# Performance work log

Hardware: AMD Instinct MI355X
Metric: run time of the kernel (lower is better)

Reference implementation:

```python
import jax, jax.numpy as jnp
import numpy as np

TEMPERATURE = 0.07
EPS = 1e-12  # F.normalize eps


def _l2norm(x):
    n = jnp.sqrt(jnp.sum(x * x, axis=-1, keepdims=True))
    return x / jnp.maximum(n, EPS)


def _nce_dir(v, x, temp):
    # Faithful to the source's bug: for every anchor k, the negative pool is the
    # FIRST N entries of the flattened (i, j!=i) negsim list, i.e.
    # sim(v0, x_j) for j=1..N-1 followed by sim(v1, x_0).
    pos = jnp.sum(v * x, axis=-1) / temp          # (N,) diagonal sims
    row0 = (v[0] @ x.T) / temp                    # (N,) sims of v0 vs all x
    extra = (v[1] @ x[0]) / temp                  # scalar: sim(v1, x0)
    sum_neg = jnp.sum(jnp.exp(row0[1:])) + jnp.exp(extra)  # fixed across k
    loss = jnp.log(jnp.exp(pos) + sum_neg) - pos  # log(sumexp_all) - log(exp_pos)
    loss = jnp.where(jnp.isnan(loss), jnp.zeros_like(loss), loss)
    return jnp.mean(loss)


def setup_inputs() -> dict:
    key = jax.random.key(0)
    k1, k2, k3 = jax.random.split(key, 3)
    N, D = 16384, 1024
    return {
        "v_f": jax.random.normal(k1, (N, D), dtype=jnp.float32),
        "a_f": jax.random.normal(k2, (N, D), dtype=jnp.float32),
        "t_f": jax.random.normal(k3, (N, D), dtype=jnp.float32),
    }


def reference(v_f, a_f, t_f):
    v = _l2norm(v_f)
    a = _l2norm(a_f)
    t = _l2norm(t_f)
    loss_va = _nce_dir(v, a, TEMPERATURE)
    loss_vt = _nce_dir(v, t, TEMPERATURE)
    return (loss_va, loss_vt)
```

## Files before the change

### kernel.cpp

```cpp
#include <hip/hip_runtime.h>
#include <math.h>

#define D_DIM 1024
#define TEMP_INV 14.285714285714286f
#define L2EPS 1e-12f

typedef float f32x4 __attribute__((ext_vector_type(4)));


__device__ __forceinline__ float dot4(const f32x4 p, const f32x4 q) {
    return p.x*q.x + p.y*q.y + p.z*q.z + p.w*q.w;
}

__global__ __launch_bounds__(256) void nce_rowstats(
    const float* __restrict__ v, const float* __restrict__ a,
    const float* __restrict__ t, float* __restrict__ ws, int N)
{
    __shared__ f32x4 v0s[256];
    const int tid  = threadIdx.x;
    const int wave = tid >> 6;
    const int lane = tid & 63;
    const int row  = blockIdx.x * 4 + wave;

    v0s[tid] = ((const f32x4*)v)[tid];
    __syncthreads();

    if (row >= N) return;

    const f32x4* vr = (const f32x4*)(v + (size_t)row * D_DIM);
    const f32x4* ar = (const f32x4*)(a + (size_t)row * D_DIM);
    const f32x4* tr = (const f32x4*)(t + (size_t)row * D_DIM);

    const f32x4 V0 = __builtin_nontemporal_load(vr + lane      );
    const f32x4 V1 = __builtin_nontemporal_load(vr + lane +  64);
    const f32x4 V2 = __builtin_nontemporal_load(vr + lane + 128);
    const f32x4 V3 = __builtin_nontemporal_load(vr + lane + 192);
    const f32x4 A0 = __builtin_nontemporal_load(ar + lane      );
    const f32x4 A1 = __builtin_nontemporal_load(ar + lane +  64);
    const f32x4 A2 = __builtin_nontemporal_load(ar + lane + 128);
    const f32x4 A3 = __builtin_nontemporal_load(ar + lane + 192);
    const f32x4 T0 = __builtin_nontemporal_load(tr + lane      );
    const f32x4 T1 = __builtin_nontemporal_load(tr + lane +  64);
    const f32x4 T2 = __builtin_nontemporal_load(tr + lane + 128);
    const f32x4 T3 = __builtin_nontemporal_load(tr + lane + 192);

    const f32x4 Z0 = v0s[lane      ];
    const f32x4 Z1 = v0s[lane +  64];
    const f32x4 Z2 = v0s[lane + 128];
    const f32x4 Z3 = v0s[lane + 192];

    float sv  = dot4(V0,V0) + dot4(V1,V1) + dot4(V2,V2) + dot4(V3,V3);
    float sa  = dot4(A0,A0) + dot4(A1,A1) + dot4(A2,A2) + dot4(A3,A3);
    float st  = dot4(T0,T0) + dot4(T1,T1) + dot4(T2,T2) + dot4(T3,T3);
    float dva = dot4(V0,A0) + dot4(V1,A1) + dot4(V2,A2) + dot4(V3,A3);
    float dvt = dot4(V0,T0) + dot4(V1,T1) + dot4(V2,T2) + dot4(V3,T3);
    float d0a = dot4(Z0,A0) + dot4(Z1,A1) + dot4(Z2,A2) + dot4(Z3,A3);
    float d0t = dot4(Z0,T0) + dot4(Z1,T1) + dot4(Z2,T2) + dot4(Z3,T3);

    #pragma unroll
    for (int off = 32; off >= 1; off >>= 1) {
        sv  += __shfl_down(sv,  off);
        sa  += __shfl_down(sa,  off);
        st  += __shfl_down(st,  off);
        dva += __shfl_down(dva, off);
        dvt += __shfl_down(dvt, off);
        d0a += __shfl_down(d0a, off);
        d0t += __shfl_down(d0t, off);
    }

    if (lane == 0) {
        ws[0*N + row] = sqrtf(sv);
        ws[1*N + row] = sqrtf(sa);
        ws[2*N + row] = sqrtf(st);
        ws[3*N + row] = dva;
        ws[4*N + row] = dvt;
        ws[5*N + row] = d0a;
        ws[6*N + row] = d0t;
    }
}

__device__ __forceinline__ void block_reduce2_256(float& x, float& y, float* sred) {
    const int lane = threadIdx.x & 63;
    const int wave = threadIdx.x >> 6;
    #pragma unroll
    for (int off = 32; off >= 1; off >>= 1) {
        x += __shfl_down(x, off);
        y += __shfl_down(y, off);
    }
    if (lane == 0) { sred[wave] = x; sred[4 + wave] = y; }
    __syncthreads();
    if (threadIdx.x == 0) {
        x = sred[0] + sred[1] + sred[2] + sred[3];
        y = sred[4] + sred[5] + sred[6] + sred[7];
    }
}

__global__ __launch_bounds__(256) void nce_partials(
    const float* __restrict__ v, const float* __restrict__ a,
    const float* __restrict__ t, float* __restrict__ ws, int N)
{
    __shared__ float sred[8];
    const int tid = threadIdx.x;
    const int bid = blockIdx.x;
    const size_t B = 7 * (size_t)N;

    float r1 = 0.f, r2 = 0.f;
    if (bid < 32) {
        const float nv0 = fmaxf(ws[0], L2EPS);
        #pragma unroll
        for (int k = 0; k < 2; ++k) {
            const int j = bid * 512 + k * 256 + tid;
            if (j == 0) continue;
            const float ia = 1.0f / (nv0 * fmaxf(ws[1*N + j], L2EPS));
            const float it = 1.0f / (nv0 * fmaxf(ws[2*N + j], L2EPS));
            r1 += expf(ws[5*N + j] * ia * TEMP_INV);
            r2 += expf(ws[6*N + j] * it * TEMP_INV);
        }
    } else {
        const f32x4 vv = *(const f32x4*)(v + D_DIM + 4 * tid);
        const f32x4 aa = *(const f32x4*)(a + 4 * tid);
        const f32x4 tt = *(const f32x4*)(t + 4 * tid);
        r1 = dot4(vv, aa);
        r2 = dot4(vv, tt);
    }
    block_reduce2_256(r1, r2, sred);
    if (tid == 0) {
        if (bid < 32) { ws[B + bid] = r1; ws[B + 32 + bid] = r2; }
        else          { ws[B + 64]  = r1; ws[B + 65]  = r2; }
    }
}

__global__ __launch_bounds__(256) void nce_loss(
    float* __restrict__ ws, int N)
{
    __shared__ float sred[8];
    const int tid = threadIdx.x;
    const int bid = blockIdx.x;
    const size_t B = 7 * (size_t)N;

    float sna = 0.f, snt = 0.f;
    #pragma unroll
    for (int i = 0; i < 32; ++i) { sna += ws[B + i]; snt += ws[B + 32 + i]; }
    const float nv1 = fmaxf(ws[0*N + 1], L2EPS);
    const float na0 = fmaxf(ws[1*N + 0], L2EPS);
    const float nt0 = fmaxf(ws[2*N + 0], L2EPS);
    const float sum_neg_a = sna + expf(ws[B + 64] / (nv1 * na0) * TEMP_INV);
    const float sum_neg_t = snt + expf(ws[B + 65] / (nv1 * nt0) * TEMP_INV);

    float la = 0.f, lt = 0.f;
    #pragma unroll
    for (int k = 0; k < 2; ++k) {
        const int kk = bid * 512 + k * 256 + tid;
        const float nvk = fmaxf(ws[0*N + kk], L2EPS);
        const float pos_a = ws[3*N + kk] / (nvk * fmaxf(ws[1*N + kk], L2EPS)) * TEMP_INV;
        const float pos_t = ws[4*N + kk] / (nvk * fmaxf(ws[2*N + kk], L2EPS)) * TEMP_INV;
        float lla = logf(expf(pos_a) + sum_neg_a) - pos_a;
        float llt = logf(expf(pos_t) + sum_neg_t) - pos_t;
        if (isnan(lla)) lla = 0.f;
        if (isnan(llt)) llt = 0.f;
        la += lla;
        lt += llt;
    }
    block_reduce2_256(la, lt, sred);
    if (tid == 0) { ws[B + 96 + bid] = la; ws[B + 128 + bid] = lt; }
}

__global__ __launch_bounds__(64) void nce_out(
    const float* __restrict__ ws, float* __restrict__ out, int N)
{
    const int lane = threadIdx.x;
    const size_t B = 7 * (size_t)N;
    float xa = (lane < 32) ? ws[B + 96 + lane]  : 0.f;
    float xt = (lane < 32) ? ws[B + 128 + lane] : 0.f;
    #pragma unroll
    for (int off = 32; off >= 1; off >>= 1) {
        xa += __shfl_down(xa, off);
        xt += __shfl_down(xt, off);
    }
    if (lane == 0) {
        out[0] = xa / (float)N;
        out[1] = xt / (float)N;
    }
}

extern "C" void kernel_launch(void* const* d_in, const int* in_sizes, int n_in,
                              void* d_out, int out_size, void* d_ws, size_t ws_size,
                              hipStream_t stream) {
    const float* v = (const float*)d_in[0];
    const float* a = (const float*)d_in[1];
    const float* t = (const float*)d_in[2];
    float* out = (float*)d_out;
    float* ws  = (float*)d_ws;
    const int N = in_sizes[0] / D_DIM;

    const int blocks = (N + 3) / 4;
    nce_rowstats<<<blocks, 256, 0, stream>>>(v, a, t, ws, N);
    nce_partials<<<33, 256, 0, stream>>>(v, a, t, ws, N);
    nce_loss<<<32, 256, 0, stream>>>(ws, N);
    nce_out<<<1, 64, 0, stream>>>(ws, out, N);
}
```

Before: 42.18 us.

## Process eight rows per wave with double-buffered inline-asm global loads

Each wave now handles eight consecutive rows instead of one. Loads for the next row are issued as raw global_load_dwordx4 instructions before the current row is computed, with an explicit s_waitcnt to keep a second buffer in flight. The shared-memory staging of v[0] is replaced by direct per-lane register loads. The grid shrinks eightfold, which cuts block-launch and row-0 reload overhead but lowers occupancy. The kernel relies on hand-written wait counts and on N being a multiple of the per-wave row count.

New measurement: 42.31 us. About the same (+0.3%).

```diff
diff --git a/kernel.cpp b/kernel.cpp
--- a/kernel.cpp
+++ b/kernel.cpp
@@ -4,6 +4,7 @@
 #define D_DIM 1024
 #define TEMP_INV 14.285714285714286f
 #define L2EPS 1e-12f
+#define RPW 8
 
 typedef float f32x4 __attribute__((ext_vector_type(4)));
 
@@ -11,71 +12,89 @@
 __device__ __forceinline__ float dot4(const f32x4 p, const f32x4 q) {
     return p.x*q.x + p.y*q.y + p.z*q.z + p.w*q.w;
 }
+
+#define GLOAD4(dst, base, imm)                                          \
+    asm volatile("global_load_dwordx4 %0, %1, off offset:" #imm         \
+                 : "=v"(dst) : "v"(base))
+#define GLOAD4NT(dst, base, imm)                                        \
+    asm volatile("global_load_dwordx4 %0, %1, off offset:" #imm " nt"   \
+                 : "=v"(dst) : "v"(base))
+
+#define ISSUE_ROW(b, vp, ap, tp)                                        \
+    do {                                                                \
+        GLOAD4NT(V[b][0], vp, 0);    GLOAD4NT(V[b][1], vp, 1024);       \
+        GLOAD4NT(V[b][2], vp, 2048); GLOAD4NT(V[b][3], vp, 3072);       \
+        GLOAD4NT(A[b][0], ap, 0);    GLOAD4NT(A[b][1], ap, 1024);       \
+        GLOAD4NT(A[b][2], ap, 2048); GLOAD4NT(A[b][3], ap, 3072);       \
+        GLOAD4NT(T[b][0], tp, 0);    GLOAD4NT(T[b][1], tp, 1024);       \
+        GLOAD4NT(T[b][2], tp, 2048); GLOAD4NT(T[b][3], tp, 3072);       \
+    } while (0)
 
 __global__ __launch_bounds__(256) void nce_rowstats(
     const float* __restrict__ v, const float* __restrict__ a,
     const float* __restrict__ t, float* __restrict__ ws, int N)
 {
-    __shared__ f32x4 v0s[256];
     const int tid  = threadIdx.x;
     const int wave = tid >> 6;
     const int lane = tid & 63;
-    const int row  = blockIdx.x * 4 + wave;
-
-    v0s[tid] = ((const f32x4*)v)[tid];
-    __syncthreads();
-
-    if (row >= N) return;
-
-    const f32x4* vr = (const f32x4*)(v + (size_t)row * D_DIM);
-    const f32x4* ar = (const f32x4*)(a + (size_t)row * D_DIM);
-    const f32x4* tr = (const f32x4*)(t + (size_t)row * D_DIM);
-
-    const f32x4 V0 = __builtin_nontemporal_load(vr + lane      );
-    const f32x4 V1 = __builtin_nontemporal_load(vr + lane +  64);
-    const f32x4 V2 = __builtin_nontemporal_load(vr + lane + 128);
-    const f32x4 V3 = __builtin_nontemporal_load(vr + lane + 192);
-    const f32x4 A0 = __builtin_nontemporal_load(ar + lane      );
-    const f32x4 A1 = __builtin_nontemporal_load(ar + lane +  64);
-    const f32x4 A2 = __builtin_nontemporal_load(ar + lane + 128);
-    const f32x4 A3 = __builtin_nontemporal_load(ar + lane + 192);
-    const f32x4 T0 = __builtin_nontemporal_load(tr + lane      );
-    const f32x4 T1 = __builtin_nontemporal_load(tr + lane +  64);
-    const f32x4 T2 = __builtin_nontemporal_load(tr + lane + 128);
-    const f32x4 T3 = __builtin_nontemporal_load(tr + lane + 192);
-
-    const f32x4 Z0 = v0s[lane      ];
-    const f32x4 Z1 = v0s[lane +  64];
-    const f32x4 Z2 = v0s[lane + 128];
-    const f32x4 Z3 = v0s[lane + 192];
-
-    float sv  = dot4(V0,V0) + dot4(V1,V1) + dot4(V2,V2) + dot4(V3,V3);
-    float sa  = dot4(A0,A0) + dot4(A1,A1) + dot4(A2,A2) + dot4(A3,A3);
-    float st  = dot4(T0,T0) + dot4(T1,T1) + dot4(T2,T2) + dot4(T3,T3);
-    float dva = dot4(V0,A0) + dot4(V1,A1) + dot4(V2,A2) + dot4(V3,A3);
-    float dvt = dot4(V0,T0) + dot4(V1,T1) + dot4(V2,T2) + dot4(V3,T3);
-    float d0a = dot4(Z0,A0) + dot4(Z1,A1) + dot4(Z2,A2) + dot4(Z3,A3);
-    float d0t = dot4(Z0,T0) + dot4(Z1,T1) + dot4(Z2,T2) + dot4(Z3,T3);
-
-    #pragma unroll
-    for (int off = 32; off >= 1; off >>= 1) {
-        sv  += __shfl_down(sv,  off);
-        sa  += __shfl_down(sa,  off);
-        st  += __shfl_down(st,  off);
-        dva += __shfl_down(dva, off);
-        dvt += __shfl_down(dvt, off);
-        d0a += __shfl_down(d0a, off);
-        d0t += __shfl_down(d0t, off);
-    }
-
-    if (lane == 0) {
-        ws[0*N + row] = sqrtf(sv);
-        ws[1*N + row] = sqrtf(sa);
-        ws[2*N + row] = sqrtf(st);
-        ws[3*N + row] = dva;
-        ws[4*N + row] = dvt;
-        ws[5*N + row] = d0a;
-        ws[6*N + row] = d0t;
+    const int wg   = blockIdx.x * 4 + wave;
+    const int row0 = wg * RPW;
+    if (row0 >= N) return;
+
+    const float* vp = v + (size_t)row0 * D_DIM + lane * 4;
+    const float* ap = a + (size_t)row0 * D_DIM + lane * 4;
+    const float* tp = t + (size_t)row0 * D_DIM + lane * 4;
+    const float* zp = v + lane * 4;
+
+    f32x4 V[2][4], A[2][4], T[2][4];
+    f32x4 Z0, Z1, Z2, Z3;
+
+    GLOAD4(Z0, zp, 0);    GLOAD4(Z1, zp, 1024);
+    GLOAD4(Z2, zp, 2048); GLOAD4(Z3, zp, 3072);
+    ISSUE_ROW(0, vp, ap, tp);
+
+    #pragma unroll
+    for (int i = 0; i < RPW; ++i) {
+        const int b  = i & 1;
+        const int nb = b ^ 1;
+        if (i + 1 < RPW) {
+            vp += D_DIM; ap += D_DIM; tp += D_DIM;
+            ISSUE_ROW(nb, vp, ap, tp);
+            asm volatile("s_waitcnt vmcnt(12)" ::: "memory");
+        } else {
+            asm volatile("s_waitcnt vmcnt(0)" ::: "memory");
+        }
+        __builtin_amdgcn_sched_barrier(0);
+
+        float sv  = dot4(V[b][0],V[b][0]) + dot4(V[b][1],V[b][1]) + dot4(V[b][2],V[b][2]) + dot4(V[b][3],V[b][3]);
+        float sa  = dot4(A[b][0],A[b][0]) + dot4(A[b][1],A[b][1]) + dot4(A[b][2],A[b][2]) + dot4(A[b][3],A[b][3]);
+        float st  = dot4(T[b][0],T[b][0]) + dot4(T[b][1],T[b][1]) + dot4(T[b][2],T[b][2]) + dot4(T[b][3],T[b][3]);
+        float dva = dot4(V[b][0],A[b][0]) + dot4(V[b][1],A[b][1]) + dot4(V[b][2],A[b][2]) + dot4(V[b][3],A[b][3]);
+        float dvt = dot4(V[b][0],T[b][0]) + dot4(V[b][1],T[b][1]) + dot4(V[b][2],T[b][2]) + dot4(V[b][3],T[b][3]);
+        float d0a = dot4(Z0,A[b][0]) + dot4(Z1,A[b][1]) + dot4(Z2,A[b][2]) + dot4(Z3,A[b][3]);
+        float d0t = dot4(Z0,T[b][0]) + dot4(Z1,T[b][1]) + dot4(Z2,T[b][2]) + dot4(Z3,T[b][3]);
+
+        #pragma unroll
+        for (int off = 32; off >= 1; off >>= 1) {
+            sv  += __shfl_down(sv,  off);
+            sa  += __shfl_down(sa,  off);
+            st  += __shfl_down(st,  off);
+            dva += __shfl_down(dva, off);
+            dvt += __shfl_down(dvt, off);
+            d0a += __shfl_down(d0a, off);
+            d0t += __shfl_down(d0t, off);
+        }
+
+        if (lane == 0) {
+            const int row = row0 + i;
+            ws[0*N + row] = sqrtf(sv);
+            ws[1*N + row] = sqrtf(sa);
+            ws[2*N + row] = sqrtf(st);
+            ws[3*N + row] = dva;
+            ws[4*N + row] = dvt;
+            ws[5*N + row] = d0a;
+            ws[6*N + row] = d0t;
+        }
     }
 }
 
@@ -193,7 +212,7 @@
     float* ws  = (float*)d_ws;
     const int N = in_sizes[0] / D_DIM;
 
-    const int blocks = (N + 3) / 4;
+    const int blocks = (N + 4 * RPW - 1) / (4 * RPW);
     nce_rowstats<<<blocks, 256, 0, stream>>>(v, a, t, ws, N);
     nce_partials<<<33, 256, 0, stream>>>(v, a, t, ws, N);
     nce_loss<<<32, 256, 0, stream>>>(ws, N);
```
